# Performance work log

Hardware: AMD Instinct MI355X
Metric: run time of the kernel (lower is better)

## Reference

```python
import jax, jax.numpy as jnp
import numpy as np

B, S, T, F = 64, 128, 64, 100
EPS = 1e-7  # K.epsilon()


def setup_inputs() -> dict:
    key = jax.random.key(0)
    ks = jax.random.split(key, 6)
    sc = 1.0 / np.sqrt(F)
    return {
        "x": jax.random.normal(ks[0], (B, S, T, F), jnp.float32),
        "W": jax.random.normal(ks[1], (F, F), jnp.float32) * sc,
        "W_context": jax.random.normal(ks[2], (F, F), jnp.float32) * sc,
        "b": jnp.zeros((F,), jnp.float32),
        "u": jax.random.normal(ks[3], (F,), jnp.float32) * sc,
        "Wx": jax.random.normal(ks[4], (F, 3 * F), jnp.float32) * sc,
        "Wh": jax.random.normal(ks[5], (F, 3 * F), jnp.float32) * sc,
        "bg": jnp.zeros((3 * F,), jnp.float32),
    }


def reference(x, W, W_context, b, u, Wx, Wh, bg):
    # x: (B, S, T, F) -> scan over sentence axis S
    Bn, Sn, Tn, Fn = x.shape

    def gru_step(h, a):
        # standard GRU cell: h (B,F), a (B,F)
        gx = a @ Wx + bg          # (B, 3F)
        gh = h @ Wh               # (B, 3F)
        zr = jax.nn.sigmoid(gx[:, : 2 * Fn] + gh[:, : 2 * Fn])
        z, r = zr[:, :Fn], zr[:, Fn:]
        h_tilde = jnp.tanh(gx[:, 2 * Fn :] + r * gh[:, 2 * Fn :])
        return (1.0 - z) * h + z * h_tilde

    def step(h, x_):
        # x_: (B, T, F); h: (B, F) recurrent context
        uit = jnp.tanh(x_ @ W + b + (h @ W_context)[:, None, :])  # (B,T,F)
        ait = uit @ u                                              # (B,T)
        a = jnp.exp(ait)
        a = a / (jnp.sum(a, axis=1, keepdims=True) + EPS)
        attended = jnp.einsum("btf,bt->bf", x_, a)                 # (B,F)
        h_new = gru_step(h, attended)
        return h_new, h_new

    h0 = jnp.zeros((Bn, Fn), x.dtype)
    _, outs = jax.lax.scan(step, h0, jnp.transpose(x, (1, 0, 2, 3)))  # (S,B,F)
    return jnp.transpose(outs, (1, 0, 2))  # (B,S,F)
```

## Files before the change

### kernel.cpp

```cpp
#include <hip/hip_runtime.h>

#define BN 64
#define SN 128
#define TN 64
#define FN 100
#define G3 300

__device__ __forceinline__ float rl(float v, int l){
  return __int_as_float(__builtin_amdgcn_readlane(__float_as_int(v), l));
}
__device__ __forceinline__ float fast_exp(float x){
  return __builtin_amdgcn_exp2f(x * 1.44269504088896341f);
}
__device__ __forceinline__ float fast_tanh(float x){
  float e = __builtin_amdgcn_exp2f(x * 2.88539008177792681f);
  return 1.0f - 2.0f * __builtin_amdgcn_rcpf(1.0f + e);
}
__device__ __forceinline__ float fast_sig(float x){
  return __builtin_amdgcn_rcpf(1.0f + __builtin_amdgcn_exp2f(-1.44269504088896341f * x));
}

__global__ __launch_bounds__(256, 3) void k_xw(
    const float* __restrict__ x, const float* __restrict__ W,
    const float* __restrict__ b, float* __restrict__ xw)
{
  const long row = (long)blockIdx.x * 256 + threadIdx.x;
  const float4* xr4 = reinterpret_cast<const float4*>(x + row * FN);
  float acc[FN];
  #pragma unroll
  for (int j = 0; j < FN; j++) acc[j] = b[j];
  #pragma unroll 1
  for (int fc = 0; fc < 25; fc++){
    float4 xv = xr4[fc];
    const float* Wr = W + fc * 4 * FN;
    #pragma unroll
    for (int j = 0; j < FN; j++) acc[j] = fmaf(xv.x, Wr[j],        acc[j]);
    #pragma unroll
    for (int j = 0; j < FN; j++) acc[j] = fmaf(xv.y, Wr[FN + j],   acc[j]);
    #pragma unroll
    for (int j = 0; j < FN; j++) acc[j] = fmaf(xv.z, Wr[2*FN + j], acc[j]);
    #pragma unroll
    for (int j = 0; j < FN; j++) acc[j] = fmaf(xv.w, Wr[3*FN + j], acc[j]);
  }
  float4* op = reinterpret_cast<float4*>(xw + row * FN);
  #pragma unroll
  for (int j = 0; j < 25; j++)
    op[j] = make_float4(acc[4*j], acc[4*j+1], acc[4*j+2], acc[4*j+3]);
}

__global__ __launch_bounds__(512, 2) void k_scan(
    const float* __restrict__ x, const float* __restrict__ xw,
    const float* __restrict__ Wc, const float* __restrict__ u,
    const float* __restrict__ Wx, const float* __restrict__ Wh,
    const float* __restrict__ bg, float* __restrict__ out)
{
  const int b    = blockIdx.x;
  const int tid  = threadIdx.x;
  const int lane = tid & 63;
  const int wid  = tid >> 6;

  const int gth = tid & 127;
  const int fsl = tid >> 7;
  const int tB  = tid >> 3;
  const int fsB = tid & 7;
  const bool fCv = (tid & 127) < FN;
  const int fC  = fCv ? (tid & 127) : (FN - 1);
  const int tsC = tid >> 7;

  __shared__ __align__(16) float xwbuf[2][TN*FN + 16];
  __shared__ float part5[700][5];
  __shared__ float h_lds[128];
  __shared__ __align__(16) float c_lds[128];
  __shared__ float att_lds[128];
  __shared__ __align__(16) float ea_lds[64];
  __shared__ float dpart[8];

  float wr[25][5];
  float wcr[25];
  const bool hasC = (gth >= 28);
  const int  co   = hasC ? gth - 28 : 0;
  #pragma unroll
  for (int j = 0; j < 25; j++){
    const int f = fsl*25 + j;
    #pragma unroll
    for (int p = 0; p < 5; p++){
      const int o = gth + 128*p;
      wr[j][p] = (o < 600) ? ((o < 300) ? Wx[f*G3 + o] : Wh[f*G3 + (o-300)]) : 0.0f;
    }
    wcr[j] = hasC ? Wc[f*FN + co] : 0.0f;
  }
  float2 ur[7];
  #pragma unroll
  for (int i = 0; i < 7; i++){
    const int f = fsB*14 + 2*i;
    ur[i].x = (f   < FN) ? u[f]   : 0.0f;
    ur[i].y = (f+1 < FN) ? u[f+1] : 0.0f;
  }
  if (tid < 128){ h_lds[tid] = 0.0f; c_lds[tid] = 0.0f; att_lds[tid] = 0.0f; }
  if (tid < 16){ xwbuf[0][TN*FN + tid] = 0.0f; xwbuf[1][TN*FN + tid] = 0.0f; }
  __syncthreads();

  const long tileStride = (long)TN*FN;
  const float* xw_base = xw + (long)b*SN*tileStride;
  const float* x_base  = x  + (long)b*SN*tileStride;

  auto issue_xw_dma = [&](int s, int bi){
    const char* g = (const char*)(xw_base + (long)s*tileStride);
    char* l = (char*)(&xwbuf[bi][0]);
    #pragma unroll
    for (int r = 0; r < 4; r++){
      const int chunk = (r*8 + wid) * 1024;
      if (chunk < 25600){
        __builtin_amdgcn_global_load_lds(
          (const __attribute__((address_space(1))) unsigned int*)(g + chunk + lane*16),
          (__attribute__((address_space(3))) unsigned int*)(l + chunk),
          16, 0, 0);
      }
    }
  };

#define ISSUE_X(sp, arr) do { \
    const float* gp_ = x_base + (long)(sp)*tileStride + (long)tsC*(16*FN) + fC; \
    _Pragma("unroll") \
    for (int k_ = 0; k_ < 16; k_++) arr[k_] = gp_[k_*FN]; \
  } while(0)

  float xcur[16], xnxt[16];
  issue_xw_dma(0, 0);
  ISSUE_X(0, xcur);

  for (int s = 0; s < SN; s++){
    float hp = h_lds[fsl*25 + (lane < 25 ? lane : 0)];
    float accC = 0.0f;
    #pragma unroll
    for (int j = 0; j < 25; j++) accC = fmaf(rl(hp, j), wcr[j], accC);
    if (hasC) part5[600 + co][fsl] = accC;
    __syncthreads();

    if (tid < FN)
      c_lds[tid] = part5[600+tid][0] + part5[600+tid][1]
                 + part5[600+tid][2] + part5[600+tid][3];
    __syncthreads();

    {
      const float2* cp  = reinterpret_cast<const float2*>(&c_lds[fsB*14]);
      const float2* xp2 = reinterpret_cast<const float2*>(&xwbuf[s&1][tB*FN + fsB*14]);
      float accB = 0.0f;
      #pragma unroll
      for (int i = 0; i < 7; i++){
        float2 cc = cp[i];
        float2 xx = xp2[i];
        accB = fmaf(fast_tanh(xx.x + cc.x), ur[i].x, accB);
        accB = fmaf(fast_tanh(xx.y + cc.y), ur[i].y, accB);
      }
      accB += __shfl_xor(accB, 1);
      accB += __shfl_xor(accB, 2);
      accB += __shfl_xor(accB, 4);
      float ea = fast_exp(accB);
      if (fsB == 0) ea_lds[tB] = ea;
      float dsum = ea;
      dsum += __shfl_xor(dsum, 8);
      dsum += __shfl_xor(dsum, 16);
      dsum += __shfl_xor(dsum, 32);
      if (lane == 0) dpart[wid] = dsum;
    }
    __syncthreads();

    {
      const float4* eap = reinterpret_cast<const float4*>(&ea_lds[tsC*16]);
      float4 e0 = eap[0], e1 = eap[1], e2 = eap[2], e3 = eap[3];
      float a = 0.0f;
      a = fmaf(xcur[0],  e0.x, a); a = fmaf(xcur[1],  e0.y, a);
      a = fmaf(xcur[2],  e0.z, a); a = fmaf(xcur[3],  e0.w, a);
      a = fmaf(xcur[4],  e1.x, a); a = fmaf(xcur[5],  e1.y, a);
      a = fmaf(xcur[6],  e1.z, a); a = fmaf(xcur[7],  e1.w, a);
      a = fmaf(xcur[8],  e2.x, a); a = fmaf(xcur[9],  e2.y, a);
      a = fmaf(xcur[10], e2.z, a); a = fmaf(xcur[11], e2.w, a);
      a = fmaf(xcur[12], e3.x, a); a = fmaf(xcur[13], e3.y, a);
      a = fmaf(xcur[14], e3.z, a); a = fmaf(xcur[15], e3.w, a);
      if (fCv) part5[600 + fC][tsC] = a;
    }
    __syncthreads();

    if (tid < FN){
      float den = dpart[0]+dpart[1]+dpart[2]+dpart[3]
                + dpart[4]+dpart[5]+dpart[6]+dpart[7] + 1e-7f;
      float sm = part5[600+tid][0]+part5[600+tid][1]
               + part5[600+tid][2]+part5[600+tid][3];
      att_lds[tid] = sm / den;
    }
    __syncthreads();

    {
      const int sp = (s+1 < SN) ? s+1 : s;
      issue_xw_dma(sp, (s+1)&1);
      ISSUE_X(sp, xnxt);
    }

    {
      float attp = att_lds[fsl*25 + (lane < 25 ? lane : 0)];
      const bool p2x = (gth < 44);
      float a0=0.f, a1=0.f, a2=0.f, a3=0.f, a4=0.f;
      #pragma unroll
      for (int j = 0; j < 25; j++){
        float sa = rl(attp, j);
        float sh = rl(hp, j);
        float s2 = p2x ? sa : sh;
        a0 = fmaf(sa, wr[j][0], a0);
        a1 = fmaf(sa, wr[j][1], a1);
        a2 = fmaf(s2, wr[j][2], a2);
        a3 = fmaf(sh, wr[j][3], a3);
        a4 = fmaf(sh, wr[j][4], a4);
      }
      part5[gth      ][fsl] = a0;
      part5[gth + 128][fsl] = a1;
      part5[gth + 256][fsl] = a2;
      part5[gth + 384][fsl] = a3;
      if (gth < 88) part5[gth + 512][fsl] = a4;
    }
    __builtin_amdgcn_s_waitcnt(0x0F70);
    __syncthreads();

    if (tid < FN){
      const int g = tid;
      float gxz = part5[g    ][0]+part5[g    ][1]+part5[g    ][2]+part5[g    ][3] + bg[g];
      float gxr = part5[100+g][0]+part5[100+g][1]+part5[100+g][2]+part5[100+g][3] + bg[100+g];
      float gxh = part5[200+g][0]+part5[200+g][1]+part5[200+g][2]+part5[200+g][3] + bg[200+g];
      float ghz = part5[300+g][0]+part5[300+g][1]+part5[300+g][2]+part5[300+g][3];
      float ghr = part5[400+g][0]+part5[400+g][1]+part5[400+g][2]+part5[400+g][3];
      float ghh = part5[500+g][0]+part5[500+g][1]+part5[500+g][2]+part5[500+g][3];
      float z  = fast_sig(gxz + ghz);
      float r  = fast_sig(gxr + ghr);
      float ht = fast_tanh(gxh + r*ghh);
      float hn = (1.0f - z)*h_lds[g] + z*ht;
      h_lds[g] = hn;
      out[((long)b*SN + s)*FN + g] = hn;
    }
    __syncthreads();
    #pragma unroll
    for (int k = 0; k < 16; k++) xcur[k] = xnxt[k];
  }
#undef ISSUE_X
}

extern "C" void kernel_launch(void* const* d_in, const int* in_sizes, int n_in,
                              void* d_out, int out_size, void* d_ws, size_t ws_size,
                              hipStream_t stream)
{
  const float* x  = (const float*)d_in[0];
  const float* W  = (const float*)d_in[1];
  const float* Wc = (const float*)d_in[2];
  const float* bb = (const float*)d_in[3];
  const float* u  = (const float*)d_in[4];
  const float* Wx = (const float*)d_in[5];
  const float* Wh = (const float*)d_in[6];
  const float* bg = (const float*)d_in[7];
  float* out = (float*)d_out;
  float* xwbuf = (float*)d_ws;

  k_xw  <<<dim3((BN*SN*TN) / 256 * 1), dim3(256), 0, stream>>>(x, W, bb, xwbuf);
  k_scan<<<dim3(BN), dim3(512), 0, stream>>>(x, xwbuf, Wc, u, Wx, Wh, bg, out);
}
```

Measured before the change: 939.5 us.

## Stage W in LDS and register-tile xW over rows and output columns

```diff
diff --git a/kernel.cpp b/kernel.cpp
--- a/kernel.cpp
+++ b/kernel.cpp
@@ -20,32 +20,80 @@
   return __builtin_amdgcn_rcpf(1.0f + __builtin_amdgcn_exp2f(-1.44269504088896341f * x));
 }
 
-__global__ __launch_bounds__(256, 3) void k_xw(
+__global__ __launch_bounds__(320, 2) void k_xw(
     const float* __restrict__ x, const float* __restrict__ W,
     const float* __restrict__ b, float* __restrict__ xw)
 {
-  const long row = (long)blockIdx.x * 256 + threadIdx.x;
-  const float4* xr4 = reinterpret_cast<const float4*>(x + row * FN);
-  float acc[FN];
+  __shared__ __align__(16) float Wl[FN * FN];
+  const int tid = threadIdx.x;
+  #pragma unroll 1
+  for (int i = tid; i < FN * FN; i += 320) Wl[i] = W[i];
+  __syncthreads();
+
+  const int lane = tid & 63;
+  const int grp  = tid >> 6;
+  const long rowbase = (long)blockIdx.x * 384;
+  const long NR = (long)BN * SN * TN;
+
+  bool vld[6];
+  const float4* xr[6];
   #pragma unroll
-  for (int j = 0; j < FN; j++) acc[j] = b[j];
+  for (int r = 0; r < 6; r++){
+    const long rr = rowbase + r * 64 + lane;
+    vld[r] = (rowbase + r * 64) < NR;
+    xr[r]  = reinterpret_cast<const float4*>(x + (vld[r] ? rr : (long)lane) * FN);
+  }
+
+  float acc[6][20];
+  {
+    const float4* bp = reinterpret_cast<const float4*>(b) + grp * 5;
+    #pragma unroll
+    for (int k = 0; k < 5; k++){
+      const float4 bv = bp[k];
+      #pragma unroll
+      for (int r = 0; r < 6; r++){
+        acc[r][4*k+0] = bv.x; acc[r][4*k+1] = bv.y;
+        acc[r][4*k+2] = bv.z; acc[r][4*k+3] = bv.w;
+      }
+    }
+  }
+
+  const float4* wb = reinterpret_cast<const float4*>(Wl) + grp * 5;
+
   #pragma unroll 1
   for (int fc = 0; fc < 25; fc++){
-    float4 xv = xr4[fc];
-    const float* Wr = W + fc * 4 * FN;
-    #pragma unroll
-    for (int j = 0; j < FN; j++) acc[j] = fmaf(xv.x, Wr[j],        acc[j]);
-    #pragma unroll
-    for (int j = 0; j < FN; j++) acc[j] = fmaf(xv.y, Wr[FN + j],   acc[j]);
-    #pragma unroll
-    for (int j = 0; j < FN; j++) acc[j] = fmaf(xv.z, Wr[2*FN + j], acc[j]);
-    #pragma unroll
-    for (int j = 0; j < FN; j++) acc[j] = fmaf(xv.w, Wr[3*FN + j], acc[j]);
-  }
-  float4* op = reinterpret_cast<float4*>(xw + row * FN);
+    float4 xv[6];
+    #pragma unroll
+    for (int r = 0; r < 6; r++) xv[r] = xr[r][fc];
+    #pragma unroll
+    for (int j = 0; j < 4; j++){
+      const float4* wr_ = wb + (4*fc + j) * 25;
+      float4 wv[5];
+      #pragma unroll
+      for (int k = 0; k < 5; k++) wv[k] = wr_[k];
+      #pragma unroll
+      for (int r = 0; r < 6; r++){
+        const float s = (j==0) ? xv[r].x : (j==1) ? xv[r].y : (j==2) ? xv[r].z : xv[r].w;
+        #pragma unroll
+        for (int k = 0; k < 5; k++){
+          acc[r][4*k+0] = fmaf(s, wv[k].x, acc[r][4*k+0]);
+          acc[r][4*k+1] = fmaf(s, wv[k].y, acc[r][4*k+1]);
+          acc[r][4*k+2] = fmaf(s, wv[k].z, acc[r][4*k+2]);
+          acc[r][4*k+3] = fmaf(s, wv[k].w, acc[r][4*k+3]);
+        }
+      }
+    }
+  }
+
   #pragma unroll
-  for (int j = 0; j < 25; j++)
-    op[j] = make_float4(acc[4*j], acc[4*j+1], acc[4*j+2], acc[4*j+3]);
+  for (int r = 0; r < 6; r++){
+    if (vld[r]){
+      float4* op = reinterpret_cast<float4*>(xw + (rowbase + r*64 + lane) * FN) + grp * 5;
+      #pragma unroll
+      for (int k = 0; k < 5; k++)
+        op[k] = make_float4(acc[r][4*k+0], acc[r][4*k+1], acc[r][4*k+2], acc[r][4*k+3]);
+    }
+  }
 }
 
 __global__ __launch_bounds__(512, 2) void k_scan(
@@ -258,6 +306,6 @@
   float* out = (float*)d_out;
   float* xwbuf = (float*)d_ws;
 
-  k_xw  <<<dim3((BN*SN*TN) / 256 * 1), dim3(256), 0, stream>>>(x, W, bb, xwbuf);
+  k_xw  <<<dim3((BN*SN*TN + 383) / 384), dim3(320), 0, stream>>>(x, W, bb, xwbuf);
   k_scan<<<dim3(BN), dim3(512), 0, stream>>>(x, xwbuf, Wc, u, Wx, Wh, bg, out);
 }
```

Result: slower. 1.151 ms (+22.5%).

## Double scan block to 1024 threads, halving per-thread serial work

Applied to the files above, without the earlier changes.

```diff
diff --git a/kernel.cpp b/kernel.cpp
--- a/kernel.cpp
+++ b/kernel.cpp
@@ -48,7 +48,7 @@
     op[j] = make_float4(acc[4*j], acc[4*j+1], acc[4*j+2], acc[4*j+3]);
 }
 
-__global__ __launch_bounds__(512, 2) void k_scan(
+__global__ __launch_bounds__(1024, 1) void k_scan(
     const float* __restrict__ x, const float* __restrict__ xw,
     const float* __restrict__ Wc, const float* __restrict__ u,
     const float* __restrict__ Wx, const float* __restrict__ Wh,
@@ -61,40 +61,40 @@
 
   const int gth = tid & 127;
   const int fsl = tid >> 7;
-  const int tB  = tid >> 3;
-  const int fsB = tid & 7;
+  const int tB  = tid >> 4;
+  const int fsB = tid & 15;
   const bool fCv = (tid & 127) < FN;
   const int fC  = fCv ? (tid & 127) : (FN - 1);
   const int tsC = tid >> 7;
 
   __shared__ __align__(16) float xwbuf[2][TN*FN + 16];
-  __shared__ float part5[700][5];
+  __shared__ float part[700][9];
   __shared__ float h_lds[128];
-  __shared__ __align__(16) float c_lds[128];
+  __shared__ float c_lds[128];
   __shared__ float att_lds[128];
   __shared__ __align__(16) float ea_lds[64];
-  __shared__ float dpart[8];
-
-  float wr[25][5];
-  float wcr[25];
+  __shared__ float dpart[16];
+
+  float wr[13][5];
+  float wcr[13];
   const bool hasC = (gth >= 28);
   const int  co   = hasC ? gth - 28 : 0;
   #pragma unroll
-  for (int j = 0; j < 25; j++){
-    const int f = fsl*25 + j;
+  for (int j = 0; j < 13; j++){
+    const int f = fsl*13 + j;
     #pragma unroll
     for (int p = 0; p < 5; p++){
       const int o = gth + 128*p;
-      wr[j][p] = (o < 600) ? ((o < 300) ? Wx[f*G3 + o] : Wh[f*G3 + (o-300)]) : 0.0f;
-    }
-    wcr[j] = hasC ? Wc[f*FN + co] : 0.0f;
-  }
-  float2 ur[7];
+      wr[j][p] = (o < 600 && f < FN)
+               ? ((o < 300) ? Wx[f*G3 + o] : Wh[f*G3 + (o-300)]) : 0.0f;
+    }
+    wcr[j] = (hasC && f < FN) ? Wc[f*FN + co] : 0.0f;
+  }
+  float ur[7];
   #pragma unroll
   for (int i = 0; i < 7; i++){
-    const int f = fsB*14 + 2*i;
-    ur[i].x = (f   < FN) ? u[f]   : 0.0f;
-    ur[i].y = (f+1 < FN) ? u[f+1] : 0.0f;
+    const int f = fsB*7 + i;
+    ur[i] = (f < FN) ? u[f] : 0.0f;
   }
   if (tid < 128){ h_lds[tid] = 0.0f; c_lds[tid] = 0.0f; att_lds[tid] = 0.0f; }
   if (tid < 16){ xwbuf[0][TN*FN + tid] = 0.0f; xwbuf[1][TN*FN + tid] = 0.0f; }
@@ -108,8 +108,8 @@
     const char* g = (const char*)(xw_base + (long)s*tileStride);
     char* l = (char*)(&xwbuf[bi][0]);
     #pragma unroll
-    for (int r = 0; r < 4; r++){
-      const int chunk = (r*8 + wid) * 1024;
+    for (int r = 0; r < 2; r++){
+      const int chunk = (r*16 + wid) * 1024;
       if (chunk < 25600){
         __builtin_amdgcn_global_load_lds(
           (const __attribute__((address_space(1))) unsigned int*)(g + chunk + lane*16),
@@ -120,46 +120,45 @@
   };
 
 #define ISSUE_X(sp, arr) do { \
-    const float* gp_ = x_base + (long)(sp)*tileStride + (long)tsC*(16*FN) + fC; \
+    const float* gp_ = x_base + (long)(sp)*tileStride + (long)tsC*(8*FN) + fC; \
     _Pragma("unroll") \
-    for (int k_ = 0; k_ < 16; k_++) arr[k_] = gp_[k_*FN]; \
+    for (int k_ = 0; k_ < 8; k_++) arr[k_] = gp_[k_*FN]; \
   } while(0)
 
-  float xcur[16], xnxt[16];
+  float xcur[8], xnxt[8];
   issue_xw_dma(0, 0);
   ISSUE_X(0, xcur);
 
   for (int s = 0; s < SN; s++){
-    float hp = h_lds[fsl*25 + (lane < 25 ? lane : 0)];
+    float hp = h_lds[fsl*13 + (lane < 13 ? lane : 0)];
     float accC = 0.0f;
     #pragma unroll
-    for (int j = 0; j < 25; j++) accC = fmaf(rl(hp, j), wcr[j], accC);
-    if (hasC) part5[600 + co][fsl] = accC;
-    __syncthreads();
-
-    if (tid < FN)
-      c_lds[tid] = part5[600+tid][0] + part5[600+tid][1]
-                 + part5[600+tid][2] + part5[600+tid][3];
-    __syncthreads();
-
-    {
-      const float2* cp  = reinterpret_cast<const float2*>(&c_lds[fsB*14]);
-      const float2* xp2 = reinterpret_cast<const float2*>(&xwbuf[s&1][tB*FN + fsB*14]);
+    for (int j = 0; j < 13; j++) accC = fmaf(rl(hp, j), wcr[j], accC);
+    if (hasC) part[600 + co][fsl] = accC;
+    __syncthreads();
+
+    if (tid < FN){
+      const float* pr = part[600 + tid];
+      c_lds[tid] = ((pr[0]+pr[1]) + (pr[2]+pr[3]))
+                 + ((pr[4]+pr[5]) + (pr[6]+pr[7]));
+    }
+    __builtin_amdgcn_s_waitcnt(0x0F70);
+    __syncthreads();
+
+    {
+      const float* cp = &c_lds[fsB*7];
+      const float* xp = &xwbuf[s&1][tB*FN + fsB*7];
       float accB = 0.0f;
       #pragma unroll
-      for (int i = 0; i < 7; i++){
-        float2 cc = cp[i];
-        float2 xx = xp2[i];
-        accB = fmaf(fast_tanh(xx.x + cc.x), ur[i].x, accB);
-        accB = fmaf(fast_tanh(xx.y + cc.y), ur[i].y, accB);
-      }
+      for (int i = 0; i < 7; i++)
+        accB = fmaf(fast_tanh(xp[i] + cp[i]), ur[i], accB);
       accB += __shfl_xor(accB, 1);
       accB += __shfl_xor(accB, 2);
       accB += __shfl_xor(accB, 4);
+      accB += __shfl_xor(accB, 8);
       float ea = fast_exp(accB);
       if (fsB == 0) ea_lds[tB] = ea;
       float dsum = ea;
-      dsum += __shfl_xor(dsum, 8);
       dsum += __shfl_xor(dsum, 16);
       dsum += __shfl_xor(dsum, 32);
       if (lane == 0) dpart[wid] = dsum;
@@ -167,26 +166,25 @@
     __syncthreads();
 
     {
-      const float4* eap = reinterpret_cast<const float4*>(&ea_lds[tsC*16]);
-      float4 e0 = eap[0], e1 = eap[1], e2 = eap[2], e3 = eap[3];
+      const float4* eap = reinterpret_cast<const float4*>(&ea_lds[tsC*8]);
+      float4 e0 = eap[0], e1 = eap[1];
       float a = 0.0f;
-      a = fmaf(xcur[0],  e0.x, a); a = fmaf(xcur[1],  e0.y, a);
-      a = fmaf(xcur[2],  e0.z, a); a = fmaf(xcur[3],  e0.w, a);
-      a = fmaf(xcur[4],  e1.x, a); a = fmaf(xcur[5],  e1.y, a);
-      a = fmaf(xcur[6],  e1.z, a); a = fmaf(xcur[7],  e1.w, a);
-      a = fmaf(xcur[8],  e2.x, a); a = fmaf(xcur[9],  e2.y, a);
-      a = fmaf(xcur[10], e2.z, a); a = fmaf(xcur[11], e2.w, a);
-      a = fmaf(xcur[12], e3.x, a); a = fmaf(xcur[13], e3.y, a);
-      a = fmaf(xcur[14], e3.z, a); a = fmaf(xcur[15], e3.w, a);
-      if (fCv) part5[600 + fC][tsC] = a;
+      a = fmaf(xcur[0], e0.x, a); a = fmaf(xcur[1], e0.y, a);
+      a = fmaf(xcur[2], e0.z, a); a = fmaf(xcur[3], e0.w, a);
+      a = fmaf(xcur[4], e1.x, a); a = fmaf(xcur[5], e1.y, a);
+      a = fmaf(xcur[6], e1.z, a); a = fmaf(xcur[7], e1.w, a);
+      if (fCv) part[600 + fC][tsC] = a;
     }
     __syncthreads();
 
     if (tid < FN){
-      float den = dpart[0]+dpart[1]+dpart[2]+dpart[3]
-                + dpart[4]+dpart[5]+dpart[6]+dpart[7] + 1e-7f;
-      float sm = part5[600+tid][0]+part5[600+tid][1]
-               + part5[600+tid][2]+part5[600+tid][3];
+      float den = ((dpart[0]+dpart[1])+(dpart[2]+dpart[3]))
+                + ((dpart[4]+dpart[5])+(dpart[6]+dpart[7]))
+                + ((dpart[8]+dpart[9])+(dpart[10]+dpart[11]))
+                + ((dpart[12]+dpart[13])+(dpart[14]+dpart[15])) + 1e-7f;
+      const float* pr = part[600 + tid];
+      float sm = ((pr[0]+pr[1]) + (pr[2]+pr[3]))
+               + ((pr[4]+pr[5]) + (pr[6]+pr[7]));
       att_lds[tid] = sm / den;
     }
     __syncthreads();
@@ -198,11 +196,11 @@
     }
 
     {
-      float attp = att_lds[fsl*25 + (lane < 25 ? lane : 0)];
+      float attp = att_lds[fsl*13 + (lane < 13 ? lane : 0)];
       const bool p2x = (gth < 44);
       float a0=0.f, a1=0.f, a2=0.f, a3=0.f, a4=0.f;
       #pragma unroll
-      for (int j = 0; j < 25; j++){
+      for (int j = 0; j < 13; j++){
         float sa = rl(attp, j);
         float sh = rl(hp, j);
         float s2 = p2x ? sa : sh;
@@ -212,23 +210,28 @@
         a3 = fmaf(sh, wr[j][3], a3);
         a4 = fmaf(sh, wr[j][4], a4);
       }
-      part5[gth      ][fsl] = a0;
-      part5[gth + 128][fsl] = a1;
-      part5[gth + 256][fsl] = a2;
-      part5[gth + 384][fsl] = a3;
-      if (gth < 88) part5[gth + 512][fsl] = a4;
-    }
-    __builtin_amdgcn_s_waitcnt(0x0F70);
+      part[gth      ][fsl] = a0;
+      part[gth + 128][fsl] = a1;
+      part[gth + 256][fsl] = a2;
+      part[gth + 384][fsl] = a3;
+      if (gth < 88) part[gth + 512][fsl] = a4;
+    }
     __syncthreads();
 
     if (tid < FN){
       const int g = tid;
-      float gxz = part5[g    ][0]+part5[g    ][1]+part5[g    ][2]+part5[g    ][3] + bg[g];
-      float gxr = part5[100+g][0]+part5[100+g][1]+part5[100+g][2]+part5[100+g][3] + bg[100+g];
-      float gxh = part5[200+g][0]+part5[200+g][1]+part5[200+g][2]+part5[200+g][3] + bg[200+g];
-      float ghz = part5[300+g][0]+part5[300+g][1]+part5[300+g][2]+part5[300+g][3];
-      float ghr = part5[400+g][0]+part5[400+g][1]+part5[400+g][2]+part5[400+g][3];
-      float ghh = part5[500+g][0]+part5[500+g][1]+part5[500+g][2]+part5[500+g][3];
+      const float* p0 = part[g];
+      const float* p1 = part[100+g];
+      const float* p2 = part[200+g];
+      const float* p3 = part[300+g];
+      const float* p4 = part[400+g];
+      const float* p5 = part[500+g];
+      float gxz = ((p0[0]+p0[1])+(p0[2]+p0[3]))+((p0[4]+p0[5])+(p0[6]+p0[7])) + bg[g];
+      float gxr = ((p1[0]+p1[1])+(p1[2]+p1[3]))+((p1[4]+p1[5])+(p1[6]+p1[7])) + bg[100+g];
+      float gxh = ((p2[0]+p2[1])+(p2[2]+p2[3]))+((p2[4]+p2[5])+(p2[6]+p2[7])) + bg[200+g];
+      float ghz = ((p3[0]+p3[1])+(p3[2]+p3[3]))+((p3[4]+p3[5])+(p3[6]+p3[7]));
+      float ghr = ((p4[0]+p4[1])+(p4[2]+p4[3]))+((p4[4]+p4[5])+(p4[6]+p4[7]));
+      float ghh = ((p5[0]+p5[1])+(p5[2]+p5[3]))+((p5[4]+p5[5])+(p5[6]+p5[7]));
       float z  = fast_sig(gxz + ghz);
       float r  = fast_sig(gxr + ghr);
       float ht = fast_tanh(gxh + r*ghh);
@@ -238,7 +241,7 @@
     }
     __syncthreads();
     #pragma unroll
-    for (int k = 0; k < 16; k++) xcur[k] = xnxt[k];
+    for (int k = 0; k < 8; k++) xcur[k] = xnxt[k];
   }
 #undef ISSUE_X
 }
@@ -258,6 +261,6 @@
   float* out = (float*)d_out;
   float* xwbuf = (float*)d_ws;
 
-  k_xw  <<<dim3((BN*SN*TN) / 256 * 1), dim3(256), 0, stream>>>(x, W, bb, xwbuf);
-  k_scan<<<dim3(BN), dim3(512), 0, stream>>>(x, xwbuf, Wc, u, Wx, Wh, bg, out);
-}
+  k_xw  <<<dim3((BN*SN*TN) / 256), dim3(256), 0, stream>>>(x, W, bb, xwbuf);
+  k_scan<<<dim3(BN), dim3(1024), 0, stream>>>(x, xwbuf, Wc, u, Wx, Wh, bg, out);
+}
```

Result: slower. 1.142 ms (+21.5%).

## Fuse x@W producer blocks into scan kernel with flag-based tile handoff

Applied to the files above, without the earlier changes.

```diff
diff --git a/kernel.cpp b/kernel.cpp
--- a/kernel.cpp
+++ b/kernel.cpp
@@ -5,6 +5,8 @@
 #define TN 64
 #define FN 100
 #define G3 300
+#define XW_BYTES 209715200L
+#define NFLAGS 2048
 
 __device__ __forceinline__ float rl(float v, int l){
   return __int_as_float(__builtin_amdgcn_readlane(__float_as_int(v), l));
@@ -22,13 +24,13 @@
 
 __global__ __launch_bounds__(256, 3) void k_xw(
     const float* __restrict__ x, const float* __restrict__ W,
-    const float* __restrict__ b, float* __restrict__ xw)
+    const float* __restrict__ bias, float* __restrict__ xw)
 {
   const long row = (long)blockIdx.x * 256 + threadIdx.x;
   const float4* xr4 = reinterpret_cast<const float4*>(x + row * FN);
   float acc[FN];
   #pragma unroll
-  for (int j = 0; j < FN; j++) acc[j] = b[j];
+  for (int j = 0; j < FN; j++) acc[j] = bias[j];
   #pragma unroll 1
   for (int fc = 0; fc < 25; fc++){
     float4 xv = xr4[fc];
@@ -48,16 +50,65 @@
     op[j] = make_float4(acc[4*j], acc[4*j+1], acc[4*j+2], acc[4*j+3]);
 }
 
-__global__ __launch_bounds__(512, 2) void k_scan(
-    const float* __restrict__ x, const float* __restrict__ xw,
+template<int OVERLAP>
+__global__ __launch_bounds__(512, 2) void k_fused(
+    const float* __restrict__ x,  const float* __restrict__ W,
+    const float* __restrict__ bias,
     const float* __restrict__ Wc, const float* __restrict__ u,
     const float* __restrict__ Wx, const float* __restrict__ Wh,
-    const float* __restrict__ bg, float* __restrict__ out)
+    const float* __restrict__ bg, float* __restrict__ xw,
+    int* __restrict__ flags,      float* __restrict__ out)
 {
-  const int b    = blockIdx.x;
   const int tid  = threadIdx.x;
   const int lane = tid & 63;
   const int wid  = tid >> 6;
+
+  if (blockIdx.x >= BN){
+    const int p    = blockIdx.x - BN;
+    const int s    = p >> 4;
+    const int q    = p & 15;
+    const int half = wid & 1;
+    const int rg   = wid >> 1;
+    const int bb   = 4*q + rg;
+    const long row = (long)bb*((long)SN*TN) + (long)s*TN + lane;
+    const float4* xr4 = reinterpret_cast<const float4*>(x + row * FN);
+    const int co = half ? 48 : 0;
+
+    float acc[52];
+    #pragma unroll
+    for (int k = 0; k < 52; k++) acc[k] = bias[co + k];
+    #pragma unroll 1
+    for (int fc = 0; fc < 25; fc++){
+      float4 xv = xr4[fc];
+      const float* Wr = W + fc*4*FN + co;
+      #pragma unroll
+      for (int k = 0; k < 52; k++) acc[k] = fmaf(xv.x, Wr[k],        acc[k]);
+      #pragma unroll
+      for (int k = 0; k < 52; k++) acc[k] = fmaf(xv.y, Wr[FN + k],   acc[k]);
+      #pragma unroll
+      for (int k = 0; k < 52; k++) acc[k] = fmaf(xv.z, Wr[2*FN + k], acc[k]);
+      #pragma unroll
+      for (int k = 0; k < 52; k++) acc[k] = fmaf(xv.w, Wr[3*FN + k], acc[k]);
+    }
+    float4* op = reinterpret_cast<float4*>(xw + row * FN);
+    if (!half){
+      #pragma unroll
+      for (int k = 0; k < 13; k++)
+        op[k] = make_float4(acc[4*k], acc[4*k+1], acc[4*k+2], acc[4*k+3]);
+    } else {
+      #pragma unroll
+      for (int k = 0; k < 12; k++)
+        op[13+k] = make_float4(acc[4+4*k], acc[5+4*k], acc[6+4*k], acc[7+4*k]);
+    }
+    __syncthreads();
+    if (tid == 0){
+      __builtin_amdgcn_fence(__ATOMIC_RELEASE, "agent");
+      __hip_atomic_store(&flags[p], 1, __ATOMIC_RELAXED, __HIP_MEMORY_SCOPE_AGENT);
+    }
+    return;
+  }
+
+  const int b = blockIdx.x;
 
   const int gth = tid & 127;
   const int fsl = tid >> 7;
@@ -96,6 +147,9 @@
     ur[i].x = (f   < FN) ? u[f]   : 0.0f;
     ur[i].y = (f+1 < FN) ? u[f+1] : 0.0f;
   }
+  float bgz = 0.0f, bgr = 0.0f, bgh = 0.0f;
+  if (tid < FN){ bgz = bg[tid]; bgr = bg[FN+tid]; bgh = bg[2*FN+tid]; }
+
   if (tid < 128){ h_lds[tid] = 0.0f; c_lds[tid] = 0.0f; att_lds[tid] = 0.0f; }
   if (tid < 16){ xwbuf[0][TN*FN + tid] = 0.0f; xwbuf[1][TN*FN + tid] = 0.0f; }
   __syncthreads();
@@ -103,6 +157,18 @@
   const long tileStride = (long)TN*FN;
   const float* xw_base = xw + (long)b*SN*tileStride;
   const float* x_base  = x  + (long)b*SN*tileStride;
+
+  auto wait_tile = [&](int s_){
+    if (OVERLAP){
+      const int* fp = flags + s_*16 + (b>>2);
+      int c = 0;
+      while (!__hip_atomic_load(fp, __ATOMIC_RELAXED, __HIP_MEMORY_SCOPE_AGENT)){
+        __builtin_amdgcn_s_sleep(16);
+        if (++c > 50000) break;
+      }
+      __builtin_amdgcn_fence(__ATOMIC_ACQUIRE, "agent");
+    }
+  };
 
   auto issue_xw_dma = [&](int s, int bi){
     const char* g = (const char*)(xw_base + (long)s*tileStride);
@@ -126,6 +192,7 @@
   } while(0)
 
   float xcur[16], xnxt[16];
+  wait_tile(0);
   issue_xw_dma(0, 0);
   ISSUE_X(0, xcur);
 
@@ -193,6 +260,7 @@
 
     {
       const int sp = (s+1 < SN) ? s+1 : s;
+      wait_tile(sp);
       issue_xw_dma(sp, (s+1)&1);
       ISSUE_X(sp, xnxt);
     }
@@ -223,9 +291,9 @@
 
     if (tid < FN){
       const int g = tid;
-      float gxz = part5[g    ][0]+part5[g    ][1]+part5[g    ][2]+part5[g    ][3] + bg[g];
-      float gxr = part5[100+g][0]+part5[100+g][1]+part5[100+g][2]+part5[100+g][3] + bg[100+g];
-      float gxh = part5[200+g][0]+part5[200+g][1]+part5[200+g][2]+part5[200+g][3] + bg[200+g];
+      float gxz = part5[g    ][0]+part5[g    ][1]+part5[g    ][2]+part5[g    ][3] + bgz;
+      float gxr = part5[100+g][0]+part5[100+g][1]+part5[100+g][2]+part5[100+g][3] + bgr;
+      float gxh = part5[200+g][0]+part5[200+g][1]+part5[200+g][2]+part5[200+g][3] + bgh;
       float ghz = part5[300+g][0]+part5[300+g][1]+part5[300+g][2]+part5[300+g][3];
       float ghr = part5[400+g][0]+part5[400+g][1]+part5[400+g][2]+part5[400+g][3];
       float ghh = part5[500+g][0]+part5[500+g][1]+part5[500+g][2]+part5[500+g][3];
@@ -257,7 +325,16 @@
   const float* bg = (const float*)d_in[7];
   float* out = (float*)d_out;
   float* xwbuf = (float*)d_ws;
-
-  k_xw  <<<dim3((BN*SN*TN) / 256 * 1), dim3(256), 0, stream>>>(x, W, bb, xwbuf);
-  k_scan<<<dim3(BN), dim3(512), 0, stream>>>(x, xwbuf, Wc, u, Wx, Wh, bg, out);
-}
+  int*   flags = (int*)((char*)d_ws + XW_BYTES);
+
+  const bool overlap = ws_size >= (size_t)XW_BYTES + NFLAGS*sizeof(int);
+  if (overlap){
+    hipMemsetAsync(flags, 0, NFLAGS*sizeof(int), stream);
+    k_fused<1><<<dim3(BN + 2048), dim3(512), 0, stream>>>(
+        x, W, bb, Wc, u, Wx, Wh, bg, xwbuf, flags, out);
+  } else {
+    k_xw<<<dim3((BN*SN*TN) / 256), dim3(256), 0, stream>>>(x, W, bb, xwbuf);
+    k_fused<0><<<dim3(BN), dim3(512), 0, stream>>>(
+        x, W, bb, Wc, u, Wx, Wh, bg, xwbuf, nullptr, out);
+  }
+}
```

Measured after the change: 1.558 ms. 1.66x slower.
